# Kernel tuning notes

Measured on AMD Instinct MI355X. Metric: run time of the kernel, lower is better.

Reference implementation:

```python
import jax, jax.numpy as jnp
import numpy as np

DIM = 128
DIM_OUT = 128
TK = 3   # time kernel (causal)
SK = 3   # spatial kernel
EPS = 1e-8


def setup_inputs() -> dict:
    key = jax.random.key(0)
    k1, k2, k3 = jax.random.split(key, 3)
    fmap = jax.random.normal(k1, (4, DIM, 16, 64, 64), dtype=jnp.float32)
    cond = jax.random.normal(k2, (4, DIM), dtype=jnp.float32)
    fan_in = DIM * TK * SK * SK
    gain = 0.75  # kaiming gain for selu
    weights = jax.random.normal(k3, (DIM_OUT, DIM, TK, SK, SK), dtype=jnp.float32) * (gain / np.sqrt(fan_in))
    return {"fmap": fmap, "cond": cond, "weights": weights}


def reference(fmap, cond, weights):
    # per-sample weight modulation: w[b,o,i,kt,kh,kw] = W[o,i,...] * (cond[b,i] + 1)
    w = weights[None] * (cond[:, None, :, None, None, None] + 1.0)
    # demodulation: normalize per (b, o) over (i, kt, kh, kw)
    ssq = jnp.sum(w * w, axis=(2, 3, 4, 5), keepdims=True)
    w = w * jax.lax.rsqrt(jnp.maximum(ssq, EPS))
    # causal time padding (TK-1, 0), symmetric spatial padding SK//2
    sp = SK // 2
    fmap_p = jnp.pad(fmap, ((0, 0), (0, 0), (TK - 1, 0), (sp, sp), (sp, sp)))
    # per-sample conv3d (equivalent to groups=b grouped conv)
    dn = ('NCDHW', 'OIDHW', 'NCDHW')
    def conv_one(x, wi):
        # x: [c, t, h, w], wi: [o, i, kt, kh, kw]
        return jax.lax.conv_general_dilated(
            x[None], wi, window_strides=(1, 1, 1), padding='VALID',
            dimension_numbers=dn)[0]
    return jax.vmap(conv_one)(fmap_p, w)  # [b, o, t, h, w]
```

## Files before the change

### kernel.cpp

```cpp
#include <hip/hip_runtime.h>

typedef float f32x4 __attribute__((ext_vector_type(4)));
typedef short s16x8 __attribute__((ext_vector_type(8)));

#define NB 4
#define CIN 128
#define COUT 128
#define NT 16
#define NH 64
#define NW 64
#define NTAP 27
#define KTOT (CIN * NTAP)

#define FT_H 66
#define FT_W 66
#define WMOD_BYTES (NB * NTAP * COUT * CIN * 2)
#define FT_U16 ((size_t)NB * NT * FT_H * FT_W * CIN)
#define FT_BYTES (FT_U16 * 2)
#define WS_NEED ((size_t)WMOD_BYTES + FT_BYTES)

#define SFT 4
#define SFH 6
#define SFW 66
#define SFPX (SFT * SFH * SFW)
#define SF_SLOTS (SFPX * 4)
#define SW_U16 (COUT * 32)

#define VMCNT1() asm volatile("s_waitcnt vmcnt(1)" ::: "memory")
#define VMCNT0() asm volatile("s_waitcnt vmcnt(0)" ::: "memory")
#define LGKM0()  asm volatile("s_waitcnt lgkmcnt(0)" ::: "memory")
#define BARRIER() asm volatile("s_barrier" ::: "memory")

__device__ __forceinline__ unsigned short f32_to_bf16(float f) {
    unsigned int u = __builtin_bit_cast(unsigned int, f);
    u += 0x7FFFu + ((u >> 16) & 1u);
    return (unsigned short)(u >> 16);
}

__device__ __forceinline__ void gload16(const void* g, void* l) {
    __builtin_amdgcn_global_load_lds(
        (const __attribute__((address_space(1))) unsigned int*)g,
        (__attribute__((address_space(3))) unsigned int*)l, 16, 0, 0);
}

__global__ __launch_bounds__(256) void modw_kernel(
    const float* __restrict__ cond,
    const float* __restrict__ weights,
    unsigned short* __restrict__ wmod,
    int swz)
{
    int bo = blockIdx.x;
    int b = bo >> 7;
    int o = bo & 127;
    int tid = threadIdx.x;
    __shared__ float red[256];
    __shared__ float s_scale;
    const float* wrow = weights + o * KTOT;
    const float* cb = cond + b * CIN;

    float acc = 0.f;
    for (int idx = tid; idx < KTOT; idx += 256) {
        int i = idx / NTAP;
        float v = wrow[idx] * (cb[i] + 1.0f);
        acc += v * v;
    }
    red[tid] = acc;
    __syncthreads();
    #pragma unroll
    for (int s = 128; s > 0; s >>= 1) {
        if (tid < s) red[tid] += red[tid + s];
        __syncthreads();
    }
    if (tid == 0) s_scale = 1.0f / sqrtf(fmaxf(red[0], 1e-8f));
    __syncthreads();
    float scale = s_scale;
    int sw_o = swz ? ((o >> 1) & 3) : 0;

    for (int idx = tid; idx < KTOT; idx += 256) {
        int i = idx / NTAP;
        int tap = idx - i * NTAP;
        float v = wrow[idx] * (cb[i] + 1.0f) * scale;
        int pos = (i & 0x60) | ((((i >> 3) & 3) ^ sw_o) << 3) | (i & 7);
        wmod[(((b * NTAP + tap) * COUT + o) * CIN) + pos] = f32_to_bf16(v);
    }
}

__global__ void border_kernel(unsigned short* __restrict__ fmapT) {
    int idx = blockIdx.x * blockDim.x + threadIdx.x;
    int total = NB * NT * 260 * 16;
    if (idx >= total) return;
    int slot = idx & 15;
    int pid = idx >> 4;
    int r = pid % 260;
    int bt = pid / 260;
    int hh, ww;
    if (r < 66)       { hh = 0;  ww = r; }
    else if (r < 132) { hh = 65; ww = r - 66; }
    else if (r < 196) { ww = 0;  hh = r - 131; }
    else              { ww = 65; hh = r - 195; }
    size_t p = (((size_t)bt * FT_H + hh) * FT_W + ww) * CIN + slot * 8;
    uint4 z = {0, 0, 0, 0};
    *reinterpret_cast<uint4*>(&fmapT[p]) = z;
}

__global__ __launch_bounds__(256) void transpose_kernel(
    const float* __restrict__ fmap, unsigned short* __restrict__ fmapT)
{
    __shared__ __attribute__((aligned(16))) unsigned short sT[NW * 136];
    int bid = blockIdx.x;
    int h = bid & 63;
    int t = (bid >> 6) & 15;
    int b = bid >> 10;
    int tid = threadIdx.x;

    int c = tid >> 1, wh = (tid & 1) * 32;
    const float* src = fmap + (((size_t)(b * CIN + c) * NT + t) * NH + h) * NW + wh;
    #pragma unroll
    for (int j = 0; j < 8; ++j) {
        float4 v = *reinterpret_cast<const float4*>(src + j * 4);
        int w = wh + j * 4;
        sT[(w + 0) * 136 + c] = f32_to_bf16(v.x);
        sT[(w + 1) * 136 + c] = f32_to_bf16(v.y);
        sT[(w + 2) * 136 + c] = f32_to_bf16(v.z);
        sT[(w + 3) * 136 + c] = f32_to_bf16(v.w);
    }
    __syncthreads();

    int w = tid >> 2, qq = tid & 3;
    int sw = ((w + 1) >> 1) & 3;
    size_t pixbase = (((size_t)(b * NT + t) * FT_H + (h + 1)) * FT_W + (w + 1)) * CIN;
    #pragma unroll
    for (int s = 0; s < 4; ++s) {
        int g = qq * 4 + s;
        uint4 v = *reinterpret_cast<const uint4*>(&sT[w * 136 + g * 8]);
        int slot = (g & 12) | ((g & 3) ^ sw);
        *reinterpret_cast<uint4*>(&fmapT[pixbase + slot * 8]) = v;
    }
}

__global__ __launch_bounds__(512, 2) void conv2_kernel(
    const unsigned short* __restrict__ fmapT,
    const unsigned short* __restrict__ wmod,
    float* __restrict__ out)
{
    __shared__ __attribute__((aligned(16))) unsigned short sF[SFPX * 32];
    __shared__ __attribute__((aligned(16))) unsigned short sW[3][SW_U16];

    int obid = blockIdx.x;
    int bid = (obid & 7) * 64 + (obid >> 3);
    int h0 = (bid & 15) * 4;
    int t0 = ((bid >> 4) & 7) * 2;
    int b  = bid >> 7;

    int tid = threadIdx.x;
    int wv = tid >> 6;
    int l  = tid & 63;
    int lo = l & 15, hi = l >> 4;
    int obase = (wv & 1) * 64;
    int tsub  = (wv >> 1) & 1;
    int hp    = (wv >> 2) * 2;

    int swzA = (lo >> 1) & 3;

    f32x4 acc[4][2][4];
    f32x4 zz = {0.f, 0.f, 0.f, 0.f};
    #pragma unroll
    for (int a = 0; a < 4; ++a)
        #pragma unroll
        for (int h2 = 0; h2 < 2; ++h2)
            #pragma unroll
            for (int p = 0; p < 4; ++p)
                acc[a][h2][p] = zz;

    int nz = (t0 == 0) ? (2 * SFH * SFW * 4) : 0;

    auto stage_f = [&](int ic) {
        #pragma unroll 1
        for (int j = 0; j < 13; ++j) {
            int s = j * 512 + tid;
            if (s < SF_SLOTS) {
                int px = s >> 2, q = s & 3;
                int row = px / SFW;
                int wl = px - row * SFW;
                int tl = row / SFH;
                int hl = row - tl * SFH;
                int ts = t0 + tl - 2;
                if (ts < 0) ts = 0;
                const unsigned short* src = fmapT +
                    ((((size_t)(b * NT + ts) * FT_H + (h0 + hl)) * FT_W + wl) << 7)
                    + (ic << 5) + (q << 3);
                gload16(src, &sF[(size_t)s * 8]);
            }
        }
    };
    auto stage_w = [&](int j) {
        if (j > 107) j = 107;
        int icw = j / 27;
        int tapw = j - icw * 27;
        const unsigned short* src = wmod +
            (((size_t)(b * NTAP + tapw) * COUT + (tid >> 2)) << 7)
            + (icw << 5) + ((tid & 3) << 3);
        gload16(src, &sW[j % 3][tid * 8]);
    };
    auto zero_t = [&]() {
        uint4 z = {0, 0, 0, 0};
        for (int s = tid; s < nz; s += 512)
            *reinterpret_cast<uint4*>(&sF[(size_t)s * 8]) = z;
    };

    stage_f(0);
    stage_w(0);
    stage_w(1);
    VMCNT0();
    if (nz) zero_t();
    LGKM0();
    BARRIER();

    int tap = 0, kt = 0, kh = 0, kw = 0, ic = 0, cur = 0;
    for (int ks = 0; ks < 108; ++ks) {
        if (tap == 0 && ks) {
            VMCNT1(); LGKM0();
            BARRIER();
            stage_f(ic);
            stage_w(ks + 2);
            VMCNT1();
            if (nz) zero_t();
            LGKM0();
            BARRIER();
        } else {
            VMCNT1(); LGKM0();
            BARRIER();
            stage_w(ks + 2);
        }

        int swzB = ((lo + kw) >> 1) & 3;
        const unsigned short* wb = &sW[cur][((obase + lo) << 5) + ((hi ^ swzA) << 3)];
        s16x8 af[4];
        #pragma unroll
        for (int a = 0; a < 4; ++a)
            af[a] = *reinterpret_cast<const s16x8*>(&wb[a << 9]);

        __builtin_amdgcn_s_setprio(1);
        #pragma unroll
        for (int h2 = 0; h2 < 2; ++h2) {
            int row = (tsub + kt) * SFH + hp + h2 + kh;
            int pix = row * SFW + kw + lo;
            const unsigned short* fb = &sF[(pix << 5) + ((hi ^ swzB) << 3)];
            s16x8 bf[4];
            #pragma unroll
            for (int p = 0; p < 4; ++p)
                bf[p] = *reinterpret_cast<const s16x8*>(&fb[p << 9]);
            #pragma unroll
            for (int a = 0; a < 4; ++a)
                #pragma unroll
                for (int p = 0; p < 4; ++p)
                    acc[a][h2][p] = __builtin_amdgcn_mfma_f32_16x16x32_bf16(
                        af[a], bf[p], acc[a][h2][p], 0, 0, 0);
        }
        __builtin_amdgcn_s_setprio(0);

        ++tap; ++kw;
        if (kw == 3) { kw = 0; ++kh; if (kh == 3) { kh = 0; ++kt; } }
        if (tap == NTAP) { tap = 0; kw = 0; kh = 0; kt = 0; ++ic; }
        cur = (cur == 2) ? 0 : cur + 1;
    }

    int t = t0 + tsub;
    #pragma unroll
    for (int a = 0; a < 4; ++a) {
        #pragma unroll
        for (int h2 = 0; h2 < 2; ++h2) {
            int h = h0 + hp + h2;
            #pragma unroll
            for (int reg = 0; reg < 4; ++reg) {
                int o = obase + a * 16 + hi * 4 + reg;
                float* orow = out + ((((size_t)b * COUT + o) * NT + t) * NH + h) * NW;
                #pragma unroll
                for (int p = 0; p < 4; ++p)
                    orow[p * 16 + lo] = acc[a][h2][p][reg];
            }
        }
    }
}

#define HB 4
#define SF_T 3
#define SF_Hf (HB + 2)
#define SF_Wf (NW + 2)
#define IPAD 40
#define SPATf (SF_T * SF_Hf * SF_Wf)

__global__ __launch_bounds__(512) void conv_kernel(
    const float* __restrict__ fmap,
    const unsigned short* __restrict__ wmod,
    float* __restrict__ out)
{
    __shared__ unsigned short sFf[SPATf * IPAD];
    __shared__ unsigned short sWf[2][COUT * IPAD];

    int bid = blockIdx.x;
    int h0 = (bid & 15) * HB;
    int t0 = (bid >> 4) & 15;
    int b  = bid >> 8;

    int tid = threadIdx.x;
    int wv = tid >> 6;
    int l  = tid & 63;
    int lo = l & 15;
    int hi = l >> 4;
    int obase = (wv & 1) * 64;
    int r = wv >> 1;

    int s_ii = tid >> 4;
    int s_ws = tid & 15;

    f32x4 acc[4][4];
    #pragma unroll
    for (int a = 0; a < 4; ++a)
        #pragma unroll
        for (int p = 0; p < 4; ++p)
            acc[a][p] = f32x4{0.f, 0.f, 0.f, 0.f};

    int tap = 0, icc = 0;
    for (int ks = 0; ks < 108; ++ks) {
        if (tap == 0) {
            if (ks) __syncthreads();
            const float* fbase = fmap + (size_t)((b * CIN + icc * 32 + s_ii) * NT) * (NH * NW);
            for (int e = s_ws; e < SPATf; e += 16) {
                int wl = e % SF_Wf;
                int rr = e / SF_Wf;
                int hl = rr % SF_Hf;
                int tl = rr / SF_Hf;
                int ts = t0 + tl - 2;
                int hs = h0 + hl - 1;
                int wsrc = wl - 1;
                float v = 0.f;
                if (ts >= 0 && (unsigned)hs < NH && (unsigned)wsrc < NW)
                    v = fbase[(ts * NH + hs) * NW + wsrc];
                sFf[e * IPAD + s_ii] = f32_to_bf16(v);
            }
            if (ks == 0) {
                int o = tid >> 2, q = tid & 3;
                const unsigned short* src =
                    wmod + (((b * NTAP + 0) * COUT + o) * CIN) + q * 8;
                *reinterpret_cast<uint4*>(&sWf[0][o * IPAD + q * 8]) =
                    *reinterpret_cast<const uint4*>(src);
            }
        }
        __syncthreads();

        if (ks + 1 < 108) {
            int ksn = ks + 1;
            int icn = ksn / 27;
            int tapn = ksn - icn * 27;
            int o = tid >> 2, q = tid & 3;
            const unsigned short* src =
                wmod + (((b * NTAP + tapn) * COUT + o) * CIN) + icn * 32 + q * 8;
            *reinterpret_cast<uint4*>(&sWf[ksn & 1][o * IPAD + q * 8]) =
                *reinterpret_cast<const uint4*>(src);
        }

        int kt = tap / 9;
        int rem = tap - kt * 9;
        int kh = rem / 3;
        int kw = rem - kh * 3;

        s16x8 af[4], bfr[4];
        #pragma unroll
        for (int a = 0; a < 4; ++a) {
            int o = obase + a * 16 + lo;
            af[a] = *reinterpret_cast<const s16x8*>(&sWf[ks & 1][o * IPAD + hi * 8]);
        }
        #pragma unroll
        for (int p = 0; p < 4; ++p) {
            int sp = (kt * SF_Hf + (r + kh)) * SF_Wf + (p * 16 + lo + kw);
            bfr[p] = *reinterpret_cast<const s16x8*>(&sFf[sp * IPAD + hi * 8]);
        }
        #pragma unroll
        for (int a = 0; a < 4; ++a)
            #pragma unroll
            for (int p = 0; p < 4; ++p)
                acc[a][p] = __builtin_amdgcn_mfma_f32_16x16x32_bf16(
                    af[a], bfr[p], acc[a][p], 0, 0, 0);

        if (++tap == 27) { tap = 0; ++icc; }
    }

    int h = h0 + r;
    #pragma unroll
    for (int a = 0; a < 4; ++a) {
        #pragma unroll
        for (int reg = 0; reg < 4; ++reg) {
            int o = obase + a * 16 + hi * 4 + reg;
            float* orow = out + ((((size_t)b * COUT + o) * NT + t0) * NH + h) * NW;
            #pragma unroll
            for (int p = 0; p < 4; ++p)
                orow[p * 16 + lo] = acc[a][p][reg];
        }
    }
}

extern "C" void kernel_launch(void* const* d_in, const int* in_sizes, int n_in,
                              void* d_out, int out_size, void* d_ws, size_t ws_size,
                              hipStream_t stream) {
    (void)in_sizes; (void)n_in; (void)out_size;
    const float* fmap    = (const float*)d_in[0];
    const float* cond    = (const float*)d_in[1];
    const float* weights = (const float*)d_in[2];
    float* outp = (float*)d_out;
    unsigned short* wmod = (unsigned short*)d_ws;

    if (ws_size >= WS_NEED) {
        unsigned short* fmapT = (unsigned short*)((char*)d_ws + WMOD_BYTES);
        modw_kernel<<<dim3(NB * COUT), dim3(256), 0, stream>>>(cond, weights, wmod, 1);
        border_kernel<<<dim3((NB * NT * 260 * 16 + 255) / 256), dim3(256), 0, stream>>>(fmapT);
        transpose_kernel<<<dim3(NB * NT * NH), dim3(256), 0, stream>>>(fmap, fmapT);
        conv2_kernel<<<dim3(NB * (NT / 2) * (NH / 4)), dim3(512), 0, stream>>>(fmapT, wmod, outp);
    } else {
        modw_kernel<<<dim3(NB * COUT), dim3(256), 0, stream>>>(cond, weights, wmod, 0);
        conv_kernel<<<dim3(NB * NT * (NH / HB)), dim3(512), 0, stream>>>(fmap, wmod, outp);
    }
}
```

Baseline: 303.2 us.

## Load modulated weights directly from global into registers, drop LDS weight staging

Removes the triple-buffered LDS staging of weights in the conv kernel. Each lane now reads its A fragments straight from global memory (with L2/L1 reuse across blocks of the same batch), and the loop is restructured into nested ic/kt/kh/kw loops with precomputed swizzle offsets. Per-tap barriers disappear and LDS use drops, so only one barrier pair per input-channel chunk remains. The cost is that global load latency now sits directly in front of the MFMAs with no prefetch. The modw_kernel layout flag changes to 0 so the weights are stored in the unswizzled layout the direct loads expect.

```diff
diff --git a/kernel.cpp b/kernel.cpp
--- a/kernel.cpp
+++ b/kernel.cpp
@@ -24,9 +24,7 @@
 #define SFW 66
 #define SFPX (SFT * SFH * SFW)
 #define SF_SLOTS (SFPX * 4)
-#define SW_U16 (COUT * 32)
-
-#define VMCNT1() asm volatile("s_waitcnt vmcnt(1)" ::: "memory")
+
 #define VMCNT0() asm volatile("s_waitcnt vmcnt(0)" ::: "memory")
 #define LGKM0()  asm volatile("s_waitcnt lgkmcnt(0)" ::: "memory")
 #define BARRIER() asm volatile("s_barrier" ::: "memory")
@@ -144,7 +142,6 @@
     float* __restrict__ out)
 {
     __shared__ __attribute__((aligned(16))) unsigned short sF[SFPX * 32];
-    __shared__ __attribute__((aligned(16))) unsigned short sW[3][SW_U16];
 
     int obid = blockIdx.x;
     int bid = (obid & 7) * 64 + (obid >> 3);
@@ -159,8 +156,6 @@
     int obase = (wv & 1) * 64;
     int tsub  = (wv >> 1) & 1;
     int hp    = (wv >> 2) * 2;
-
-    int swzA = (lo >> 1) & 3;
 
     f32x4 acc[4][2][4];
     f32x4 zz = {0.f, 0.f, 0.f, 0.f};
@@ -193,76 +188,67 @@
             }
         }
     };
-    auto stage_w = [&](int j) {
-        if (j > 107) j = 107;
-        int icw = j / 27;
-        int tapw = j - icw * 27;
-        const unsigned short* src = wmod +
-            (((size_t)(b * NTAP + tapw) * COUT + (tid >> 2)) << 7)
-            + (icw << 5) + ((tid & 3) << 3);
-        gload16(src, &sW[j % 3][tid * 8]);
-    };
     auto zero_t = [&]() {
         uint4 z = {0, 0, 0, 0};
         for (int s = tid; s < nz; s += 512)
             *reinterpret_cast<uint4*>(&sF[(size_t)s * 8]) = z;
     };
 
-    stage_f(0);
-    stage_w(0);
-    stage_w(1);
-    VMCNT0();
-    if (nz) zero_t();
-    LGKM0();
-    BARRIER();
-
-    int tap = 0, kt = 0, kh = 0, kw = 0, ic = 0, cur = 0;
-    for (int ks = 0; ks < 108; ++ks) {
-        if (tap == 0 && ks) {
-            VMCNT1(); LGKM0();
-            BARRIER();
-            stage_f(ic);
-            stage_w(ks + 2);
-            VMCNT1();
-            if (nz) zero_t();
+    const unsigned short* wlane = wmod
+        + ((size_t)b * NTAP * COUT) * CIN
+        + (obase + lo) * CIN + hi * 8;
+
+    int offk[3];
+    #pragma unroll
+    for (int kw = 0; kw < 3; ++kw)
+        offk[kw] = ((kw + lo) << 5) + ((hi ^ (((lo + kw) >> 1) & 3)) << 3);
+
+    #pragma unroll 1
+    for (int ic = 0; ic < 4; ++ic) {
+        if (ic) {
             LGKM0();
             BARRIER();
-        } else {
-            VMCNT1(); LGKM0();
-            BARRIER();
-            stage_w(ks + 2);
-        }
-
-        int swzB = ((lo + kw) >> 1) & 3;
-        const unsigned short* wb = &sW[cur][((obase + lo) << 5) + ((hi ^ swzA) << 3)];
-        s16x8 af[4];
-        #pragma unroll
-        for (int a = 0; a < 4; ++a)
-            af[a] = *reinterpret_cast<const s16x8*>(&wb[a << 9]);
-
-        __builtin_amdgcn_s_setprio(1);
-        #pragma unroll
-        for (int h2 = 0; h2 < 2; ++h2) {
-            int row = (tsub + kt) * SFH + hp + h2 + kh;
-            int pix = row * SFW + kw + lo;
-            const unsigned short* fb = &sF[(pix << 5) + ((hi ^ swzB) << 3)];
-            s16x8 bf[4];
+        }
+        stage_f(ic);
+        VMCNT0();
+        if (nz) zero_t();
+        LGKM0();
+        BARRIER();
+
+        const unsigned short* wch = wlane + (ic << 5);
+        #pragma unroll 1
+        for (int kt = 0; kt < 3; ++kt) {
+            const unsigned short* wkt = wch + (size_t)kt * 9 * COUT * CIN;
+            int rb = ((tsub + kt) * SFH + hp) * (SFW * 32);
             #pragma unroll
-            for (int p = 0; p < 4; ++p)
-                bf[p] = *reinterpret_cast<const s16x8*>(&fb[p << 9]);
-            #pragma unroll
-            for (int a = 0; a < 4; ++a)
+            for (int kh = 0; kh < 3; ++kh) {
                 #pragma unroll
-                for (int p = 0; p < 4; ++p)
-                    acc[a][h2][p] = __builtin_amdgcn_mfma_f32_16x16x32_bf16(
-                        af[a], bf[p], acc[a][h2][p], 0, 0, 0);
-        }
-        __builtin_amdgcn_s_setprio(0);
-
-        ++tap; ++kw;
-        if (kw == 3) { kw = 0; ++kh; if (kh == 3) { kh = 0; ++kt; } }
-        if (tap == NTAP) { tap = 0; kw = 0; kh = 0; kt = 0; ++ic; }
-        cur = (cur == 2) ? 0 : cur + 1;
+                for (int kw = 0; kw < 3; ++kw) {
+                    const unsigned short* wtap = wkt + (kh * 3 + kw) * (COUT * CIN);
+                    s16x8 af[4];
+                    #pragma unroll
+                    for (int a = 0; a < 4; ++a)
+                        af[a] = *reinterpret_cast<const s16x8*>(wtap + a * 16 * CIN);
+
+                    __builtin_amdgcn_s_setprio(1);
+                    #pragma unroll
+                    for (int h2 = 0; h2 < 2; ++h2) {
+                        int eb = rb + (h2 + kh) * (SFW * 32) + offk[kw];
+                        s16x8 bf[4];
+                        #pragma unroll
+                        for (int p = 0; p < 4; ++p)
+                            bf[p] = *reinterpret_cast<const s16x8*>(&sF[eb + p * 512]);
+                        #pragma unroll
+                        for (int a = 0; a < 4; ++a)
+                            #pragma unroll
+                            for (int p = 0; p < 4; ++p)
+                                acc[a][h2][p] = __builtin_amdgcn_mfma_f32_16x16x32_bf16(
+                                    af[a], bf[p], acc[a][h2][p], 0, 0, 0);
+                    }
+                    __builtin_amdgcn_s_setprio(0);
+                }
+            }
+        }
     }
 
     int t = t0 + tsub;
@@ -412,7 +398,7 @@
 
     if (ws_size >= WS_NEED) {
         unsigned short* fmapT = (unsigned short*)((char*)d_ws + WMOD_BYTES);
-        modw_kernel<<<dim3(NB * COUT), dim3(256), 0, stream>>>(cond, weights, wmod, 1);
+        modw_kernel<<<dim3(NB * COUT), dim3(256), 0, stream>>>(cond, weights, wmod, 0);
         border_kernel<<<dim3((NB * NT * 260 * 16 + 255) / 256), dim3(256), 0, stream>>>(fmapT);
         transpose_kernel<<<dim3(NB * NT * NH), dim3(256), 0, stream>>>(fmap, fmapT);
         conv2_kernel<<<dim3(NB * (NT / 2) * (NH / 4)), dim3(512), 0, stream>>>(fmapT, wmod, outp);
```

Result: no change. 302.0 us (-0.4%).
